# Optimization experiments

Hardware: AMD Instinct MI355X
Metric: run time of the kernel (lower is better)

The kernel has to match this reference:

```python
import jax, jax.numpy as jnp
import numpy as np

# Module hyperparameters (match torch init_kwargs)
D_MODEL = 512
N_HEADS = 8
WINDOW_LEN = 128
DIL_FACTOR = 64
N_DIL = 2
ATTN_SINK = True
SRC_LEN = 2048
BSZ = 2


def setup_inputs() -> dict:
    key = jax.random.key(0)
    ks = jax.random.split(key, 6)
    w_scale = 0.04  # ~ xavier_uniform scale for 512x512
    inp = {
        "x": jax.random.normal(ks[0], (SRC_LEN, BSZ, D_MODEL), jnp.float32),
        "Wq": jax.random.normal(ks[1], (D_MODEL, D_MODEL), jnp.float32) * w_scale,
        "bq": jnp.zeros((D_MODEL,), jnp.float32),
        "Wk": jax.random.normal(ks[2], (D_MODEL, D_MODEL), jnp.float32) * w_scale,
        "bk": jnp.zeros((D_MODEL,), jnp.float32),
        "Wv": jax.random.normal(ks[3], (D_MODEL, D_MODEL), jnp.float32) * w_scale,
        "bv": jnp.zeros((D_MODEL,), jnp.float32),
        "Wo": jax.random.normal(ks[4], (D_MODEL, D_MODEL), jnp.float32) * w_scale,
        "bo": jnp.zeros((D_MODEL,), jnp.float32),
        "beta": jnp.zeros((N_HEADS,), jnp.float32),
    }
    return inp


def _fast_attention(x, Wq, bq, Wk, bk, Wv, bv, Wo, bo, beta):
    s, b, dm = x.shape  # (src_len, bsz, d_model)
    h = N_HEADS
    d = dm // h
    q = x @ Wq.T + bq
    k = x @ Wk.T + bk
    v = x @ Wv.T + bv

    def split_heads(t):  # 's b (h d) -> (b h) s d'
        return t.reshape(s, b, h, d).transpose(1, 2, 0, 3).reshape(b * h, s, d)

    q, k, v = split_heads(q), split_heads(k), split_heads(v)

    # beta: per-head temperature, tiled over batch (matches torch .repeat(bsz,1,1))
    beta_e = jnp.tile(jnp.exp(beta), b)[:, None, None]  # (b*h, 1, 1)
    q = q / (jnp.sqrt(jnp.asarray(d, q.dtype)) * beta_e)

    attn_out = jnp.zeros_like(v)
    z = b * h
    for i in range(N_DIL):
        dil = DIL_FACTOR ** i
        p = (WINDOW_LEN - 1) * dil
        pad = (p % s) if (p % s) != p else 0  # static python ints
        nw = pad // dil + 1  # num windows
        # causal left-padded strided windowed view of q: (z, nw, s, d)
        qp = jnp.pad(q, ((0, 0), (pad, 0), (0, 0)))
        idx = (jnp.arange(nw) * dil)[:, None] + jnp.arange(s)[None, :]  # (nw, s)
        qi = qp[:, idx, :]
        w = jnp.einsum('zbsd,zsd->zbs', qi, k)  # (z, nw, s)
        if ATTN_SINK:
            w = jnp.concatenate([w, jnp.zeros((z, 1, s), w.dtype)], axis=1)
        w = jax.nn.softmax(w, axis=1)  # softmax over window axis (+ sink)
        if ATTN_SINK:
            w = w[:, :-1]
        k2 = jnp.einsum('zbs,zsd->zbd', w, k)  # (z, nw, d)
        v2 = jnp.einsum('zbs,zsd->zbd', w, v)
        # left-pad back to full length (zeros at front, values at end)
        k = jnp.pad(k2, ((0, 0), (s - nw, 0), (0, 0)))
        v = jnp.pad(v2, ((0, 0), (s - nw, 0), (0, 0)))
        attn_out = attn_out + v

    # '(b h) s d -> s b (h d)'
    out = attn_out.reshape(b, h, s, d).transpose(2, 0, 1, 3).reshape(s, b, dm)
    return out @ Wo.T + bo


def reference(x, Wq, bq, Wk, bk, Wv, bv, Wo, bo, beta):
    return _fast_attention(x, Wq, bq, Wk, bk, Wv, bv, Wo, bo, beta)
```

## Files before the change

kernel.cpp:

```cpp
#include <hip/hip_runtime.h>
#include <math.h>

#define S_LEN 2048
#define BSZ 2
#define DM 512
#define NH 8
#define HD 64
#define RTOT (S_LEN*BSZ)
#define T_KEEP 32
#define ROW0 ((S_LEN - T_KEEP)*BSZ)
#define NXELEM (RTOT*DM)
#define NWROW  (NH*128)
#define NWELEM (NWROW*DM)

typedef __attribute__((ext_vector_type(8))) _Float16 half8;
typedef __attribute__((ext_vector_type(4))) float floatx4;

__device__ __forceinline__ void gld16(const void* g, void* l) {
    __builtin_amdgcn_global_load_lds((const __attribute__((address_space(1))) void*)g,
                                     (__attribute__((address_space(3))) void*)l, 16, 0, 0);
}

__device__ __forceinline__ short cvt1(float v) {
    _Float16 h = (_Float16)v;
    return __builtin_bit_cast(short, h);
}

__global__ __launch_bounds__(256) void convert(
    const float* __restrict__ x,
    const float* __restrict__ Wq, const float* __restrict__ Wk,
    const float* __restrict__ bo,
    short* __restrict__ xf, short* __restrict__ wf,
    float* __restrict__ sbar, float* __restrict__ Ssum,
    float* __restrict__ out)
{
    const int g = blockIdx.x*blockDim.x + threadIdx.x;
    const int stride = gridDim.x*blockDim.x;
    const int total4 = (NXELEM + NWELEM)/4;
    for (int i = g; i < total4; i += stride) {
        float4 v; size_t dst; short* d;
        if (i < NXELEM/4) {
            v = ((const float4*)x)[i];
            dst = (size_t)i*4; d = xf;
        } else {
            int e = (i - NXELEM/4)*4;
            int R = e >> 9;
            int k = e & 511;
            int h = R >> 7;
            int p = R & 127;
            int m = p >> 6;
            int c = p & 63;
            const float* W = m ? Wk : Wq;
            v = *(const float4*)&W[(size_t)(h*HD + c)*DM + k];
            dst = (size_t)R*DM + k; d = wf;
        }
        short4 hv;
        hv.x = cvt1(v.x); hv.y = cvt1(v.y); hv.z = cvt1(v.z); hv.w = cvt1(v.w);
        *(short4*)&d[dst] = hv;
    }
    {
        const float4* b4 = (const float4*)bo;
        float4* o4 = (float4*)out;
        const int fill4 = ROW0*DM/4;
        for (int i = g; i < fill4; i += stride) o4[i] = b4[i & 127];
    }
    if (g < 16*DM) sbar[g] = 0.f;
    if (g < 16)    Ssum[g] = 0.f;
}

__global__ __launch_bounds__(256, 1) void qk_sig(
    const _Float16* __restrict__ xf, const _Float16* __restrict__ wf,
    const float* __restrict__ x,
    const float* __restrict__ bq, const float* __restrict__ bk,
    const float* __restrict__ beta,
    float* __restrict__ sbar, float* __restrict__ Ssum,
    float* __restrict__ qsel)
{
    __shared__ __align__(16) char smem[65536];

    const int tid  = threadIdx.x;
    const int w    = tid >> 6;
    const int lane = tid & 63;
    const int lrow = lane & 15;
    const int lk8  = lane >> 4;
    const int bid  = blockIdx.x;
    const int rc   = (bid & 7)*4 + (bid >> 6);
    const int h    = (bid >> 3) & 7;
    const int r0   = rc * 128;

    const int jsub  = lk8;
    const int sslot = lrow ^ (jsub << 2);
    const _Float16* wsrc = wf + (size_t)(h*128 + w*32 + jsub)*DM + sslot*8;

    #pragma unroll
    for (int i = 0; i < 8; ++i)
        gld16(wsrc + (size_t)(4*i)*DM, smem + (w*8 + i)*1024);

    const int rbA = r0 + w*16;
    const int rbB = r0 + (w+4)*16;
    const _Float16* paA = xf + (size_t)(rbA + lrow)*DM + lk8*8;
    const _Float16* paB = xf + (size_t)(rbB + lrow)*DM + lk8*8;

    floatx4 acc[2][8];
    #pragma unroll
    for (int jt = 0; jt < 8; ++jt) { acc[0][jt] = (floatx4)0.f; acc[1][jt] = (floatx4)0.f; }

    half8 Aa[2][4], Ab[2][4];
    #pragma unroll
    for (int kc2 = 0; kc2 < 4; ++kc2) {
        Aa[0][kc2] = *(const half8*)(paA + kc2*32);
        Ab[0][kc2] = *(const half8*)(paB + kc2*32);
    }

    __syncthreads();

    #pragma unroll
    for (int kq = 0; kq < 4; ++kq) {
        const int cur = kq & 1, nxt = cur ^ 1;
        if (kq < 3) {
            #pragma unroll
            for (int kc2 = 0; kc2 < 4; ++kc2) {
                Aa[nxt][kc2] = *(const half8*)(paA + ((kq+1)*4 + kc2)*32);
                Ab[nxt][kc2] = *(const half8*)(paB + ((kq+1)*4 + kc2)*32);
            }
            char* nb = smem + nxt*32768;
            #pragma unroll
            for (int i = 0; i < 8; ++i)
                gld16(wsrc + (size_t)(4*i)*DM + (kq+1)*128, nb + (w*8 + i)*1024);
        }
        const char* buf = smem + cur*32768;
        #pragma unroll
        for (int kc2 = 0; kc2 < 4; ++kc2) {
            #pragma unroll
            for (int jt = 0; jt < 8; ++jt) {
                const int j = jt*16 + lrow;
                const int slotp = (kc2*4 + lk8) ^ ((lrow & 3) << 2);
                half8 bf = *(const half8*)(buf + j*256 + slotp*16);
                acc[0][jt] = __builtin_amdgcn_mfma_f32_16x16x32_f16(Aa[cur][kc2], bf, acc[0][jt], 0, 0, 0);
                acc[1][jt] = __builtin_amdgcn_mfma_f32_16x16x32_f16(Ab[cur][kc2], bf, acc[1][jt], 0, 0, 0);
            }
        }
        __syncthreads();
    }

    float* s_sig = (float*)smem;
    float bqv[4], bkv[4];
    #pragma unroll
    for (int jt = 0; jt < 4; ++jt) {
        bqv[jt] = bq[h*HD + jt*16 + lrow];
        bkv[jt] = bk[h*HD + jt*16 + lrow];
    }
    const float isc = 1.0f / (8.0f * expf(beta[h]));

    #pragma unroll
    for (int t = 0; t < 2; ++t) {
        #pragma unroll
        for (int r = 0; r < 4; ++r) {
            float q[4]; float p = 0.f;
            #pragma unroll
            for (int jt = 0; jt < 4; ++jt) {
                float qv = acc[t][jt][r]   + bqv[jt];
                float kv = acc[t][jt+4][r] + bkv[jt];
                q[jt] = qv;
                p += qv * kv;
            }
            p += __shfl_xor(p, 1, 64);
            p += __shfl_xor(p, 2, 64);
            p += __shfl_xor(p, 4, 64);
            p += __shfl_xor(p, 8, 64);
            const int rowl = (w + t*4)*16 + lk8*4 + r;
            if (lrow == 0)
                s_sig[rowl] = 1.0f / (1.0f + expf(-p * isc));
            if (rowl >= 126) {
                const int b = rowl & 1;
                float* qd = &qsel[((size_t)((b*NH + h)*T_KEEP) + rc)*64];
                #pragma unroll
                for (int jt = 0; jt < 4; ++jt) qd[jt*16 + lrow] = q[jt];
            }
        }
    }
    __syncthreads();

    {
        const int b  = tid & 1;
        const int cg = tid >> 1;
        const float* px = x + (size_t)(r0 + b)*DM + cg*4;
        float a0=0.f, a1=0.f, a2=0.f, a3=0.f;
        #pragma unroll 8
        for (int si = 0; si < 64; ++si) {
            const float sg = s_sig[si*2 + b];
            const float4 xv = *(const float4*)(px + (size_t)(si*2)*DM);
            a0 += sg*xv.x; a1 += sg*xv.y; a2 += sg*xv.z; a3 += sg*xv.w;
        }
        float* sd = &sbar[(size_t)(b*NH + h)*DM + cg*4];
        atomicAdd(sd+0, a0); atomicAdd(sd+1, a1);
        atomicAdd(sd+2, a2); atomicAdd(sd+3, a3);
    }
    if (tid < 2) {
        float s = 0.f;
        for (int i = 0; i < 64; ++i) s += s_sig[i*2 + tid];
        atomicAdd(&Ssum[tid*NH + h], s);
    }
}

__global__ __launch_bounds__(256) void kvbar_coef(
    const float* __restrict__ sbar, const float* __restrict__ Ssum,
    const float* __restrict__ Wk, const float* __restrict__ bk,
    const float* __restrict__ Wv, const float* __restrict__ bv,
    const float* __restrict__ qsel, const float* __restrict__ beta,
    float* __restrict__ vbar, float* __restrict__ coef)
{
    const int z  = blockIdx.x >> 1;
    const int kv = blockIdx.x & 1;
    const int h  = z & 7;
    const int tid = threadIdx.x;

    __shared__ float s_sb[DM];
    __shared__ float s_red[64][4];
    __shared__ float s_kb[64];
    __shared__ float s_part[T_KEEP][8];

    s_sb[tid]       = sbar[z*DM + tid];
    s_sb[tid + 256] = sbar[z*DM + 256 + tid];
    __syncthreads();
    const float S = Ssum[z];

    const float* W    = kv ? Wv : Wk;
    const float* bvec = kv ? bv : bk;
    {
        const int j = tid >> 2, kp = tid & 3;
        const float* wr = &W[(size_t)(h*HD + j)*DM + kp*128];
        float a = 0.f;
        #pragma unroll
        for (int k = 0; k < 128; k += 4) {
            float4 w4 = *(const float4*)&wr[k];
            int k0 = kp*128 + k;
            a += w4.x*s_sb[k0] + w4.y*s_sb[k0+1] + w4.z*s_sb[k0+2] + w4.w*s_sb[k0+3];
        }
        s_red[j][kp] = a;
    }
    __syncthreads();
    if (tid < 64) {
        float val = s_red[tid][0]+s_red[tid][1]+s_red[tid][2]+s_red[tid][3]
                  + bvec[h*HD + tid]*S;
        if (kv) vbar[z*HD + tid] = val;
        else    s_kb[tid] = val;
    }
    if (kv) return;
    __syncthreads();
    {
        const int wi = tid >> 3, jg = tid & 7;
        const float* qrow = &qsel[((size_t)z*T_KEEP + wi)*64 + jg*8];
        float4 q1 = *(const float4*)qrow;
        float4 q2 = *(const float4*)(qrow + 4);
        const int j0 = jg*8;
        float p = q1.x*s_kb[j0]   + q1.y*s_kb[j0+1] + q1.z*s_kb[j0+2] + q1.w*s_kb[j0+3]
                + q2.x*s_kb[j0+4] + q2.y*s_kb[j0+5] + q2.z*s_kb[j0+6] + q2.w*s_kb[j0+7];
        s_part[wi][jg] = p;
    }
    __syncthreads();
    if (tid < T_KEEP) {
        float sc = 0.f;
        #pragma unroll
        for (int gg = 0; gg < 8; ++gg) sc += s_part[tid][gg];
        sc *= 1.0f / (8.0f * expf(beta[h]));
        float m = sc;
        #pragma unroll
        for (int off = 16; off > 0; off >>= 1) m = fmaxf(m, __shfl_xor(m, off, 64));
        m = fmaxf(m, 0.f);
        float e = expf(sc - m);
        float d = e;
        #pragma unroll
        for (int off = 16; off > 0; off >>= 1) d += __shfl_xor(d, off, 64);
        d += expf(-m);
        float c = e / d;
        if (tid == T_KEEP-1) c += 1.0f;
        coef[z*T_KEEP + tid] = c;
    }
}

__global__ __launch_bounds__(256) void gout(
    const float* __restrict__ coef, const float* __restrict__ vbar,
    const float* __restrict__ Wo, const float* __restrict__ bo,
    float* __restrict__ out)
{
    const int b  = blockIdx.x & 1;
    const int cc = blockIdx.x >> 1;
    const int tid = threadIdx.x;

    __shared__ float s_cf[NH][T_KEEP];
    __shared__ float s_vb[NH*HD];
    __shared__ float s_gp[16][NH][2];

    s_vb[tid]       = vbar[b*512 + tid];
    s_vb[tid + 256] = vbar[b*512 + 256 + tid];
    s_cf[tid >> 5][tid & 31] = coef[((size_t)(b*NH) + (tid >> 5))*T_KEEP + (tid & 31)];
    __syncthreads();

    {
        const int ci = tid & 15, hh = (tid >> 4) & 7, j2 = tid >> 7;
        const float* wr = &Wo[(size_t)(cc*16 + ci)*DM + hh*HD + j2*32];
        const float* vb = &s_vb[hh*HD + j2*32];
        float a = 0.f;
        #pragma unroll
        for (int j = 0; j < 32; j += 4) {
            float4 w4 = *(const float4*)&wr[j];
            a += w4.x*vb[j] + w4.y*vb[j+1] + w4.z*vb[j+2] + w4.w*vb[j+3];
        }
        s_gp[ci][hh][j2] = a;
    }
    __syncthreads();
    {
        const int ci = tid & 15;
        const float bov = bo[cc*16 + ci];
        #pragma unroll
        for (int hf = 0; hf < 2; ++hf) {
            const int wi = (tid >> 4) + hf*16;
            float v = bov;
            #pragma unroll
            for (int hh = 0; hh < NH; ++hh)
                v += s_cf[hh][wi] * (s_gp[ci][hh][0] + s_gp[ci][hh][1]);
            out[(size_t)(ROW0 + wi*2 + b)*DM + cc*16 + ci] = v;
        }
    }
}

extern "C" void kernel_launch(void* const* d_in, const int* in_sizes, int n_in,
                              void* d_out, int out_size, void* d_ws, size_t ws_size,
                              hipStream_t stream) {
    const float* x    = (const float*)d_in[0];
    const float* Wq   = (const float*)d_in[1];
    const float* bq   = (const float*)d_in[2];
    const float* Wk   = (const float*)d_in[3];
    const float* bk   = (const float*)d_in[4];
    const float* Wv   = (const float*)d_in[5];
    const float* bv   = (const float*)d_in[6];
    const float* Wo   = (const float*)d_in[7];
    const float* bo   = (const float*)d_in[8];
    const float* beta = (const float*)d_in[9];

    char* ws = (char*)d_ws;
    float* qsel = (float*)(ws + 0);
    float* sbar = (float*)(ws + 131072);
    float* Ssum = (float*)(ws + 163840);
    float* coef = (float*)(ws + 164096);
    float* vbar = (float*)(ws + 166144);
    short* xf   = (short*)(ws + 262144);
    short* wf   = (short*)(ws + 262144 + 4194304);
    float* out  = (float*)d_out;

    convert<<<2048, 256, 0, stream>>>(x, Wq, Wk, bo, xf, wf, sbar, Ssum, out);
    qk_sig<<<256, 256, 0, stream>>>((const _Float16*)xf, (const _Float16*)wf, x,
                                    bq, bk, beta, sbar, Ssum, qsel);
    kvbar_coef<<<32, 256, 0, stream>>>(sbar, Ssum, Wk, bk, Wv, bv, qsel, beta, vbar, coef);
    gout<<<64, 256, 0, stream>>>(coef, vbar, Wo, bo, out);
}
```

Baseline: 113.4 us.

## Fuse fp16 conversion into GEMM kernel and merge tail kernels, drop atomics

Removes the separate conversion pass: the main MFMA kernel now loads fp32 x and W directly, converts them to fp16 in registers and stages W into LDS with an XOR swizzle, while also filling the bias rows of the output. Atomic accumulation of sbar/Ssum is replaced by per-block partial buffers, which a single merged tail kernel reduces before computing k/v bars, softmax coefficients and the output projection. This drops the write and re-read of the fp16 copies and cuts four launches to two. In exchange, each block re-reads fp32 weights (twice the bytes), direct LDS loads are replaced by register-staged stores, and the tail redundantly recomputes kbar/vbar in every block.

```diff
diff --git a/kernel.cpp b/kernel.cpp
--- a/kernel.cpp
+++ b/kernel.cpp
@@ -9,72 +9,24 @@
 #define RTOT (S_LEN*BSZ)
 #define T_KEEP 32
 #define ROW0 ((S_LEN - T_KEEP)*BSZ)
-#define NXELEM (RTOT*DM)
-#define NWROW  (NH*128)
-#define NWELEM (NWROW*DM)
 
 typedef __attribute__((ext_vector_type(8))) _Float16 half8;
 typedef __attribute__((ext_vector_type(4))) float floatx4;
 
-__device__ __forceinline__ void gld16(const void* g, void* l) {
-    __builtin_amdgcn_global_load_lds((const __attribute__((address_space(1))) void*)g,
-                                     (__attribute__((address_space(3))) void*)l, 16, 0, 0);
+__device__ __forceinline__ half8 pack8(float4 a, float4 b) {
+    half8 h;
+    h[0]=(_Float16)a.x; h[1]=(_Float16)a.y; h[2]=(_Float16)a.z; h[3]=(_Float16)a.w;
+    h[4]=(_Float16)b.x; h[5]=(_Float16)b.y; h[6]=(_Float16)b.z; h[7]=(_Float16)b.w;
+    return h;
 }
 
-__device__ __forceinline__ short cvt1(float v) {
-    _Float16 h = (_Float16)v;
-    return __builtin_bit_cast(short, h);
-}
-
-__global__ __launch_bounds__(256) void convert(
+__global__ __launch_bounds__(256, 1) void mega(
     const float* __restrict__ x,
     const float* __restrict__ Wq, const float* __restrict__ Wk,
-    const float* __restrict__ bo,
-    short* __restrict__ xf, short* __restrict__ wf,
-    float* __restrict__ sbar, float* __restrict__ Ssum,
-    float* __restrict__ out)
-{
-    const int g = blockIdx.x*blockDim.x + threadIdx.x;
-    const int stride = gridDim.x*blockDim.x;
-    const int total4 = (NXELEM + NWELEM)/4;
-    for (int i = g; i < total4; i += stride) {
-        float4 v; size_t dst; short* d;
-        if (i < NXELEM/4) {
-            v = ((const float4*)x)[i];
-            dst = (size_t)i*4; d = xf;
-        } else {
-            int e = (i - NXELEM/4)*4;
-            int R = e >> 9;
-            int k = e & 511;
-            int h = R >> 7;
-            int p = R & 127;
-            int m = p >> 6;
-            int c = p & 63;
-            const float* W = m ? Wk : Wq;
-            v = *(const float4*)&W[(size_t)(h*HD + c)*DM + k];
-            dst = (size_t)R*DM + k; d = wf;
-        }
-        short4 hv;
-        hv.x = cvt1(v.x); hv.y = cvt1(v.y); hv.z = cvt1(v.z); hv.w = cvt1(v.w);
-        *(short4*)&d[dst] = hv;
-    }
-    {
-        const float4* b4 = (const float4*)bo;
-        float4* o4 = (float4*)out;
-        const int fill4 = ROW0*DM/4;
-        for (int i = g; i < fill4; i += stride) o4[i] = b4[i & 127];
-    }
-    if (g < 16*DM) sbar[g] = 0.f;
-    if (g < 16)    Ssum[g] = 0.f;
-}
-
-__global__ __launch_bounds__(256, 1) void qk_sig(
-    const _Float16* __restrict__ xf, const _Float16* __restrict__ wf,
-    const float* __restrict__ x,
     const float* __restrict__ bq, const float* __restrict__ bk,
-    const float* __restrict__ beta,
-    float* __restrict__ sbar, float* __restrict__ Ssum,
-    float* __restrict__ qsel)
+    const float* __restrict__ beta, const float* __restrict__ bo,
+    float* __restrict__ spart, float* __restrict__ ssump,
+    float* __restrict__ qsel, float* __restrict__ out)
 {
     __shared__ __align__(16) char smem[65536];
 
@@ -88,56 +40,97 @@
     const int h    = (bid >> 3) & 7;
     const int r0   = rc * 128;
 
-    const int jsub  = lk8;
-    const int sslot = lrow ^ (jsub << 2);
-    const _Float16* wsrc = wf + (size_t)(h*128 + w*32 + jsub)*DM + sslot*8;
-
-    #pragma unroll
-    for (int i = 0; i < 8; ++i)
-        gld16(wsrc + (size_t)(4*i)*DM, smem + (w*8 + i)*1024);
-
-    const int rbA = r0 + w*16;
-    const int rbB = r0 + (w+4)*16;
-    const _Float16* paA = xf + (size_t)(rbA + lrow)*DM + lk8*8;
-    const _Float16* paB = xf + (size_t)(rbB + lrow)*DM + lk8*8;
+    {
+        const float4* b4 = (const float4*)bo;
+        float4* o4 = (float4*)out + (size_t)bid*2016;
+        const int base = bid*2016;
+        #pragma unroll
+        for (int i = 0; i < 8; ++i) {
+            int idx = i*256 + tid;
+            if (idx < 2016) o4[idx] = b4[(base + idx) & 127];
+        }
+    }
+
+    const int jsub = lk8;
+    const int l15  = lrow;
+
+    #pragma unroll
+    for (int i = 0; i < 8; ++i) {
+        const int chunk = w*8 + i;
+        const int j = chunk*4 + jsub;
+        const int s = l15 ^ (j & 15);
+        const float* src = (j < 64 ? Wq + (size_t)(h*HD + j)*DM
+                                   : Wk + (size_t)(h*HD + j - 64)*DM) + s*8;
+        float4 f0 = *(const float4*)src;
+        float4 f1 = *(const float4*)(src + 4);
+        *(half8*)(smem + chunk*1024 + jsub*256 + l15*16) = pack8(f0, f1);
+    }
+
+    const float* xA = x + (size_t)(r0 + w*16 + lrow)*DM + lk8*8;
+    const float* xB = x + (size_t)(r0 + (w+4)*16 + lrow)*DM + lk8*8;
+
+    half8 Aa[4], Ab[4];
+    #pragma unroll
+    for (int kc2 = 0; kc2 < 4; ++kc2) {
+        Aa[kc2] = pack8(*(const float4*)(xA + kc2*32), *(const float4*)(xA + kc2*32 + 4));
+        Ab[kc2] = pack8(*(const float4*)(xB + kc2*32), *(const float4*)(xB + kc2*32 + 4));
+    }
 
     floatx4 acc[2][8];
     #pragma unroll
     for (int jt = 0; jt < 8; ++jt) { acc[0][jt] = (floatx4)0.f; acc[1][jt] = (floatx4)0.f; }
 
-    half8 Aa[2][4], Ab[2][4];
-    #pragma unroll
-    for (int kc2 = 0; kc2 < 4; ++kc2) {
-        Aa[0][kc2] = *(const half8*)(paA + kc2*32);
-        Ab[0][kc2] = *(const half8*)(paB + kc2*32);
-    }
-
     __syncthreads();
 
     #pragma unroll
     for (int kq = 0; kq < 4; ++kq) {
-        const int cur = kq & 1, nxt = cur ^ 1;
+        const char* buf = smem + (kq & 1)*32768;
+        char* nb = smem + ((kq + 1) & 1)*32768;
+
+        float4 AF[8], BF[8], WF0[8], WF1[8];
         if (kq < 3) {
             #pragma unroll
             for (int kc2 = 0; kc2 < 4; ++kc2) {
-                Aa[nxt][kc2] = *(const half8*)(paA + ((kq+1)*4 + kc2)*32);
-                Ab[nxt][kc2] = *(const half8*)(paB + ((kq+1)*4 + kc2)*32);
-            }
-            char* nb = smem + nxt*32768;
-            #pragma unroll
-            for (int i = 0; i < 8; ++i)
-                gld16(wsrc + (size_t)(4*i)*DM + (kq+1)*128, nb + (w*8 + i)*1024);
-        }
-        const char* buf = smem + cur*32768;
+                AF[kc2*2]   = *(const float4*)(xA + (kq+1)*128 + kc2*32);
+                AF[kc2*2+1] = *(const float4*)(xA + (kq+1)*128 + kc2*32 + 4);
+                BF[kc2*2]   = *(const float4*)(xB + (kq+1)*128 + kc2*32);
+                BF[kc2*2+1] = *(const float4*)(xB + (kq+1)*128 + kc2*32 + 4);
+            }
+            #pragma unroll
+            for (int i = 0; i < 8; ++i) {
+                const int chunk = w*8 + i;
+                const int j = chunk*4 + jsub;
+                const int s = l15 ^ (j & 15);
+                const float* src = (j < 64 ? Wq + (size_t)(h*HD + j)*DM
+                                           : Wk + (size_t)(h*HD + j - 64)*DM)
+                                   + (kq+1)*128 + s*8;
+                WF0[i] = *(const float4*)src;
+                WF1[i] = *(const float4*)(src + 4);
+            }
+        }
+
         #pragma unroll
         for (int kc2 = 0; kc2 < 4; ++kc2) {
             #pragma unroll
             for (int jt = 0; jt < 8; ++jt) {
                 const int j = jt*16 + lrow;
-                const int slotp = (kc2*4 + lk8) ^ ((lrow & 3) << 2);
+                const int slotp = (kc2*4 + lk8) ^ lrow;
                 half8 bf = *(const half8*)(buf + j*256 + slotp*16);
-                acc[0][jt] = __builtin_amdgcn_mfma_f32_16x16x32_f16(Aa[cur][kc2], bf, acc[0][jt], 0, 0, 0);
-                acc[1][jt] = __builtin_amdgcn_mfma_f32_16x16x32_f16(Ab[cur][kc2], bf, acc[1][jt], 0, 0, 0);
+                acc[0][jt] = __builtin_amdgcn_mfma_f32_16x16x32_f16(Aa[kc2], bf, acc[0][jt], 0, 0, 0);
+                acc[1][jt] = __builtin_amdgcn_mfma_f32_16x16x32_f16(Ab[kc2], bf, acc[1][jt], 0, 0, 0);
+            }
+        }
+
+        if (kq < 3) {
+            #pragma unroll
+            for (int kc2 = 0; kc2 < 4; ++kc2) {
+                Aa[kc2] = pack8(AF[kc2*2], AF[kc2*2+1]);
+                Ab[kc2] = pack8(BF[kc2*2], BF[kc2*2+1]);
+            }
+            #pragma unroll
+            for (int i = 0; i < 8; ++i) {
+                const int chunk = w*8 + i;
+                *(half8*)(nb + chunk*1024 + jsub*256 + l15*16) = pack8(WF0[i], WF1[i]);
             }
         }
         __syncthreads();
@@ -192,109 +185,109 @@
             const float4 xv = *(const float4*)(px + (size_t)(si*2)*DM);
             a0 += sg*xv.x; a1 += sg*xv.y; a2 += sg*xv.z; a3 += sg*xv.w;
         }
-        float* sd = &sbar[(size_t)(b*NH + h)*DM + cg*4];
-        atomicAdd(sd+0, a0); atomicAdd(sd+1, a1);
-        atomicAdd(sd+2, a2); atomicAdd(sd+3, a3);
+        float4 st; st.x = a0; st.y = a1; st.z = a2; st.w = a3;
+        *(float4*)&spart[((size_t)(rc*2 + b)*8 + h)*512 + cg*4] = st;
     }
     if (tid < 2) {
         float s = 0.f;
         for (int i = 0; i < 64; ++i) s += s_sig[i*2 + tid];
-        atomicAdd(&Ssum[tid*NH + h], s);
+        ssump[(rc*2 + tid)*8 + h] = s;
     }
 }
 
-__global__ __launch_bounds__(256) void kvbar_coef(
-    const float* __restrict__ sbar, const float* __restrict__ Ssum,
+__global__ __launch_bounds__(256) void tail(
+    const float* __restrict__ spart, const float* __restrict__ ssump,
+    const float* __restrict__ qsel, const float* __restrict__ beta,
     const float* __restrict__ Wk, const float* __restrict__ bk,
     const float* __restrict__ Wv, const float* __restrict__ bv,
-    const float* __restrict__ qsel, const float* __restrict__ beta,
-    float* __restrict__ vbar, float* __restrict__ coef)
+    const float* __restrict__ Wo, const float* __restrict__ bo,
+    float* __restrict__ out)
 {
-    const int z  = blockIdx.x >> 1;
-    const int kv = blockIdx.x & 1;
-    const int h  = z & 7;
+    const int bidx = blockIdx.x;
+    const int b  = bidx & 1;
+    const int cc = bidx >> 1;
     const int tid = threadIdx.x;
 
-    __shared__ float s_sb[DM];
-    __shared__ float s_red[64][4];
-    __shared__ float s_kb[64];
-    __shared__ float s_part[T_KEEP][8];
-
-    s_sb[tid]       = sbar[z*DM + tid];
-    s_sb[tid + 256] = sbar[z*DM + 256 + tid];
-    __syncthreads();
-    const float S = Ssum[z];
-
-    const float* W    = kv ? Wv : Wk;
-    const float* bvec = kv ? bv : bk;
-    {
-        const int j = tid >> 2, kp = tid & 3;
-        const float* wr = &W[(size_t)(h*HD + j)*DM + kp*128];
-        float a = 0.f;
-        #pragma unroll
-        for (int k = 0; k < 128; k += 4) {
-            float4 w4 = *(const float4*)&wr[k];
-            int k0 = kp*128 + k;
-            a += w4.x*s_sb[k0] + w4.y*s_sb[k0+1] + w4.z*s_sb[k0+2] + w4.w*s_sb[k0+3];
-        }
-        s_red[j][kp] = a;
-    }
-    __syncthreads();
-    if (tid < 64) {
-        float val = s_red[tid][0]+s_red[tid][1]+s_red[tid][2]+s_red[tid][3]
-                  + bvec[h*HD + tid]*S;
-        if (kv) vbar[z*HD + tid] = val;
-        else    s_kb[tid] = val;
-    }
-    if (kv) return;
-    __syncthreads();
-    {
-        const int wi = tid >> 3, jg = tid & 7;
-        const float* qrow = &qsel[((size_t)z*T_KEEP + wi)*64 + jg*8];
-        float4 q1 = *(const float4*)qrow;
-        float4 q2 = *(const float4*)(qrow + 4);
-        const int j0 = jg*8;
-        float p = q1.x*s_kb[j0]   + q1.y*s_kb[j0+1] + q1.z*s_kb[j0+2] + q1.w*s_kb[j0+3]
-                + q2.x*s_kb[j0+4] + q2.y*s_kb[j0+5] + q2.z*s_kb[j0+6] + q2.w*s_kb[j0+7];
-        s_part[wi][jg] = p;
-    }
-    __syncthreads();
-    if (tid < T_KEEP) {
-        float sc = 0.f;
-        #pragma unroll
-        for (int gg = 0; gg < 8; ++gg) sc += s_part[tid][gg];
-        sc *= 1.0f / (8.0f * expf(beta[h]));
-        float m = sc;
+    __shared__ float s_sb[NH*DM];
+    __shared__ float s_S[NH];
+    __shared__ float s_kb[NH*HD];
+    __shared__ float s_vb[NH*HD];
+    __shared__ float s_cf[NH*T_KEEP];
+    __shared__ float s_gp[16][NH][2];
+
+    #pragma unroll
+    for (int g = 0; g < 4; ++g) {
+        const int fidx = g*256 + tid;
+        const int hh = fidx >> 7;
+        const int c4 = fidx & 127;
+        float a0=0.f, a1=0.f, a2=0.f, a3=0.f;
+        for (int rcc = 0; rcc < 32; ++rcc) {
+            float4 v = *(const float4*)&spart[((size_t)(rcc*2 + b)*8 + hh)*512 + c4*4];
+            a0 += v.x; a1 += v.y; a2 += v.z; a3 += v.w;
+        }
+        float4 st; st.x = a0; st.y = a1; st.z = a2; st.w = a3;
+        *(float4*)&s_sb[fidx*4] = st;
+    }
+    if (tid < NH) {
+        float s = 0.f;
+        for (int rcc = 0; rcc < 32; ++rcc) s += ssump[(rcc*2 + b)*8 + tid];
+        s_S[tid] = s;
+    }
+    __syncthreads();
+
+    {
+        const int hh = tid >> 5;
+        const int jq = tid & 31;
+        const float* wk0 = &Wk[(size_t)(hh*HD + jq)*DM];
+        const float* wk1 = &Wk[(size_t)(hh*HD + jq + 32)*DM];
+        const float* wv0 = &Wv[(size_t)(hh*HD + jq)*DM];
+        const float* wv1 = &Wv[(size_t)(hh*HD + jq + 32)*DM];
+        const float* sb  = &s_sb[hh*DM];
+        float ak0=0.f, ak1=0.f, av0=0.f, av1=0.f;
+        for (int k = 0; k < DM; k += 4) {
+            float4 s4 = *(const float4*)&sb[k];
+            float4 a4 = *(const float4*)&wk0[k];
+            float4 b4 = *(const float4*)&wk1[k];
+            float4 c4 = *(const float4*)&wv0[k];
+            float4 d4 = *(const float4*)&wv1[k];
+            ak0 += a4.x*s4.x + a4.y*s4.y + a4.z*s4.z + a4.w*s4.w;
+            ak1 += b4.x*s4.x + b4.y*s4.y + b4.z*s4.z + b4.w*s4.w;
+            av0 += c4.x*s4.x + c4.y*s4.y + c4.z*s4.z + c4.w*s4.w;
+            av1 += d4.x*s4.x + d4.y*s4.y + d4.z*s4.z + d4.w*s4.w;
+        }
+        const float S = s_S[hh];
+        s_kb[hh*HD + jq]      = ak0 + bk[hh*HD + jq]*S;
+        s_kb[hh*HD + jq + 32] = ak1 + bk[hh*HD + jq + 32]*S;
+        s_vb[hh*HD + jq]      = av0 + bv[hh*HD + jq]*S;
+        s_vb[hh*HD + jq + 32] = av1 + bv[hh*HD + jq + 32]*S;
+    }
+    __syncthreads();
+
+    {
+        const int hh = tid >> 5;
+        const int wi = tid & 31;
+        const float* qrow = &qsel[(((size_t)(b*NH + hh))*T_KEEP + wi)*64];
+        const float* kb = &s_kb[hh*HD];
+        float p = 0.f;
+        #pragma unroll
+        for (int j = 0; j < 64; j += 4) {
+            float4 q4 = *(const float4*)&qrow[j];
+            p += q4.x*kb[j] + q4.y*kb[j+1] + q4.z*kb[j+2] + q4.w*kb[j+3];
+        }
+        p *= 1.0f / (8.0f * expf(beta[hh]));
+        float m = p;
         #pragma unroll
         for (int off = 16; off > 0; off >>= 1) m = fmaxf(m, __shfl_xor(m, off, 64));
         m = fmaxf(m, 0.f);
-        float e = expf(sc - m);
+        float e = expf(p - m);
         float d = e;
         #pragma unroll
         for (int off = 16; off > 0; off >>= 1) d += __shfl_xor(d, off, 64);
         d += expf(-m);
         float c = e / d;
-        if (tid == T_KEEP-1) c += 1.0f;
-        coef[z*T_KEEP + tid] = c;
-    }
-}
-
-__global__ __launch_bounds__(256) void gout(
-    const float* __restrict__ coef, const float* __restrict__ vbar,
-    const float* __restrict__ Wo, const float* __restrict__ bo,
-    float* __restrict__ out)
-{
-    const int b  = blockIdx.x & 1;
-    const int cc = blockIdx.x >> 1;
-    const int tid = threadIdx.x;
-
-    __shared__ float s_cf[NH][T_KEEP];
-    __shared__ float s_vb[NH*HD];
-    __shared__ float s_gp[16][NH][2];
-
-    s_vb[tid]       = vbar[b*512 + tid];
-    s_vb[tid + 256] = vbar[b*512 + 256 + tid];
-    s_cf[tid >> 5][tid & 31] = coef[((size_t)(b*NH) + (tid >> 5))*T_KEEP + (tid & 31)];
+        if (wi == T_KEEP-1) c += 1.0f;
+        s_cf[hh*T_KEEP + wi] = c;
+    }
     __syncthreads();
 
     {
@@ -319,7 +312,7 @@
             float v = bov;
             #pragma unroll
             for (int hh = 0; hh < NH; ++hh)
-                v += s_cf[hh][wi] * (s_gp[ci][hh][0] + s_gp[ci][hh][1]);
+                v += s_cf[hh*T_KEEP + wi] * (s_gp[ci][hh][0] + s_gp[ci][hh][1]);
             out[(size_t)(ROW0 + wi*2 + b)*DM + cc*16 + ci] = v;
         }
     }
@@ -340,18 +333,13 @@
     const float* beta = (const float*)d_in[9];
 
     char* ws = (char*)d_ws;
-    float* qsel = (float*)(ws + 0);
-    float* sbar = (float*)(ws + 131072);
-    float* Ssum = (float*)(ws + 163840);
-    float* coef = (float*)(ws + 164096);
-    float* vbar = (float*)(ws + 166144);
-    short* xf   = (short*)(ws + 262144);
-    short* wf   = (short*)(ws + 262144 + 4194304);
-    float* out  = (float*)d_out;
-
-    convert<<<2048, 256, 0, stream>>>(x, Wq, Wk, bo, xf, wf, sbar, Ssum, out);
-    qk_sig<<<256, 256, 0, stream>>>((const _Float16*)xf, (const _Float16*)wf, x,
-                                    bq, bk, beta, sbar, Ssum, qsel);
-    kvbar_coef<<<32, 256, 0, stream>>>(sbar, Ssum, Wk, bk, Wv, bv, qsel, beta, vbar, coef);
-    gout<<<64, 256, 0, stream>>>(coef, vbar, Wo, bo, out);
+    float* spart = (float*)(ws + 0);
+    float* ssump = (float*)(ws + 1048576);
+    float* qsel  = (float*)(ws + 1052672);
+    float* out   = (float*)d_out;
+
+    mega<<<256, 256, 0, stream>>>(x, Wq, Wk, bq, bk, beta, bo,
+                                  spart, ssump, qsel, out);
+    tail<<<64, 256, 0, stream>>>(spart, ssump, qsel, beta,
+                                 Wk, bk, Wv, bv, Wo, bo, out);
 }
```

New measurement: 173.3 us. 1.53x slower.
